# Kernel optimization log

Measured on AMD Instinct MI355X. Metric: run time of the kernel, lower is better.

## Reference

```python
import jax, jax.numpy as jnp
import numpy as np

B, L, D = 4, 4096, 1024


def setup_inputs() -> dict:
    key = jax.random.key(0)
    ks = jax.random.split(key, 10)
    s = 1.0 / np.sqrt(D)  # torch Linear default init scale
    return {
        "x": jax.random.normal(ks[0], (B, L, D), dtype=jnp.float32),
        "hidden": jax.random.normal(ks[1], (B, D), dtype=jnp.float32),
        "W_ln_z": jax.random.uniform(ks[2], (D, D), jnp.float32, -s, s),
        "b_ln_z": jax.random.uniform(ks[3], (D,), jnp.float32, -s, s),
        "W_dt": jax.random.uniform(ks[4], (D, D), jnp.float32, -s, s),
        "b_dt": jax.random.uniform(ks[5], (D,), jnp.float32, -s, s),
        "W_y": jax.random.uniform(ks[6], (D, D), jnp.float32, -s, s),
        "b_y": jax.random.uniform(ks[7], (D,), jnp.float32, -s, s),
        "W_g": jax.random.uniform(ks[8], (D, D), jnp.float32, -s, s),
        "b_g": jax.random.uniform(ks[9], (D,), jnp.float32, -s, s),
    }


def reference(x, hidden, W_ln_z, b_ln_z, W_dt, b_dt, W_y, b_y, W_g, b_g):
    # Linear projections (torch Linear: x @ W.T + b)
    z_pre = x @ W_ln_z.T + b_ln_z          # (B, L, D)
    dt_pre = x @ W_dt.T + b_dt             # (B, L, D)

    # -softplus(-u) == log_sigmoid(u)
    ln_z = jax.nn.log_sigmoid(z_pre)       # ln z
    ln_da = jax.nn.log_sigmoid(dt_pre)     # ln(delta*a)
    ln_z_da = ln_z + ln_da
    ln_o_da = jax.nn.log_sigmoid(-dt_pre)  # -softplus(dt_pre)

    ln_o_da_cumsum = jnp.cumsum(ln_o_da, axis=1)
    # log-space parallel scan: h_t = sum_{s<=t} z_s*da_s * prod_{s<r<=t} o_da_r
    lcse = jax.lax.cumlogsumexp(ln_z_da - ln_o_da_cumsum, axis=1)
    h_inner = jnp.exp(lcse + ln_o_da_cumsum)                       # (B, L, D)
    h_cross = jnp.exp(ln_o_da_cumsum) * hidden[:, None, :]         # (B, L, D)
    h = h_inner + h_cross

    gate = jax.nn.silu(x @ W_g.T + b_g)
    y = (h @ W_y.T + b_y) * gate
    return y, h
```

## Files before the change

kernel.cpp:

```cpp
#include <hip/hip_runtime.h>


#define BDIM 4
#define LDIM 4096
#define DDIM 1024
#define MROWS (BDIM * LDIM)
#define KDIM 1024
#define NPROJ 3072
#define NCHUNK 64
#define LCHUNK 64

typedef __attribute__((ext_vector_type(8))) short short8v;
typedef __attribute__((ext_vector_type(4))) float f32x4;
typedef unsigned int uint;

__device__ __forceinline__ float bf2f(short u) {
    union { float f; uint i; } v;
    v.i = ((uint)(unsigned short)u) << 16;
    return v.f;
}
__device__ __forceinline__ short f2bf(float f) {
    union { float f; uint i; } v; v.f = f;
    uint r = v.i + 0x7FFFu + ((v.i >> 16) & 1u);
    return (short)(r >> 16);
}
__device__ __forceinline__ float sigf(float x) { return 1.f / (1.f + __expf(-x)); }

#define SCANSTEP(zz, dd, H0, H1, A0, A1, DO_A)                                     \
  {                                                                                \
    float _z0 = bf2f((short)((zz) & 0xffff)), _z1 = bf2f((short)((zz) >> 16));     \
    float _d0 = bf2f((short)((dd) & 0xffff)), _d1 = bf2f((short)((dd) >> 16));     \
    float _e0 = __expf(-_d0), _r0 = 1.f / (1.f + _e0);                             \
    float _o0 = _e0 * _r0, _q0 = sigf(_z0) * _r0;                                  \
    float _e1 = __expf(-_d1), _r1 = 1.f / (1.f + _e1);                             \
    float _o1 = _e1 * _r1, _q1 = sigf(_z1) * _r1;                                  \
    H0 = _q0 + _o0 * H0; H1 = _q1 + _o1 * H1;                                      \
    if (DO_A) { A0 *= _o0; A1 *= _o1; }                                            \
  }

__global__ __launch_bounds__(256) void fused_init(
    const float* __restrict__ x,
    const float* __restrict__ W_ln_z, const float* __restrict__ W_dt,
    const float* __restrict__ W_g,    const float* __restrict__ W_y,
    const float* __restrict__ b_ln_z, const float* __restrict__ b_dt,
    const float* __restrict__ b_g,
    short* __restrict__ x_bf, short* __restrict__ Wcat, float* __restrict__ biascat)
{
    int i = blockIdx.x * blockDim.x + threadIdx.x;
    if (i < 4194304) {
        float4 v = reinterpret_cast<const float4*>(x)[i];
        short4 o;
        o.x = f2bf(v.x); o.y = f2bf(v.y); o.z = f2bf(v.z); o.w = f2bf(v.w);
        reinterpret_cast<short4*>(x_bf)[i] = o;
    } else if (i < 5242880) {
        int j = i - 4194304;
        int seg = j >> 18, off = j & ((1 << 18) - 1);
        const float* s = (seg == 0) ? W_ln_z : (seg == 1) ? W_dt : (seg == 2) ? W_g : W_y;
        float4 v = reinterpret_cast<const float4*>(s)[off];
        short4 o;
        o.x = f2bf(v.x); o.y = f2bf(v.y); o.z = f2bf(v.z); o.w = f2bf(v.w);
        reinterpret_cast<short4*>(Wcat)[j] = o;
    } else if (i < 5243648) {
        int j = i - 5242880;
        int seg = j >> 8, off = j & 255;
        const float* s = (seg == 0) ? b_ln_z : (seg == 1) ? b_dt : b_g;
        reinterpret_cast<float4*>(biascat)[j] =
            reinterpret_cast<const float4*>(s)[off];
    }
}

#define STAGE(arr, gbase, half, kofs)                                              \
  do {                                                                             \
    _Pragma("unroll")                                                              \
    for (int _i = 0; _i < 2; ++_i) {                                               \
      int _c = _i * 512 + tid;                                                     \
      int _row = _c >> 3, _g = _c & 7;                                             \
      int _gsw = _g ^ (_row & 7);                                                  \
      __builtin_amdgcn_global_load_lds(                                            \
        (const __attribute__((address_space(1))) void*)(                           \
            (gbase) + (size_t)((half) * 128 + _row) * K + (kofs) + _gsw * 8),      \
        (__attribute__((address_space(3))) void*)(                                 \
            &arr[(_i * 512 + wid * 64) * 8]),                                      \
        16, 0, 0);                                                                 \
    }                                                                              \
  } while (0)

#define LDA4(dst, arr)                                                             \
  _Pragma("unroll")                                                                \
  for (int _m = 0; _m < 4; ++_m) {                                                 \
    int _r = _m * 32 + wm * 16 + lrow;                                             \
    _Pragma("unroll")                                                              \
    for (int _kk = 0; _kk < 2; ++_kk)                                              \
      dst[_m][_kk] = *(const short8v*)&arr[_r * 64 +                               \
                       (((_kk * 4 + kq) ^ (lrow & 7)) * 8)];                       \
  }

#define LDB2(dst, arr)                                                             \
  _Pragma("unroll")                                                                \
  for (int _n = 0; _n < 2; ++_n) {                                                 \
    int _r = _n * 64 + wn * 16 + lrow;                                             \
    _Pragma("unroll")                                                              \
    for (int _kk = 0; _kk < 2; ++_kk)                                              \
      dst[_n][_kk] = *(const short8v*)&arr[_r * 64 +                               \
                       (((_kk * 4 + kq) ^ (lrow & 7)) * 8)];                       \
  }

#define MFMAQ(mi0, ni0, afr, bfr)                                                  \
  __builtin_amdgcn_s_setprio(1);                                                   \
  _Pragma("unroll")                                                                \
  for (int _kk = 0; _kk < 2; ++_kk)                                                \
    _Pragma("unroll")                                                              \
    for (int _m = 0; _m < 4; ++_m)                                                 \
      _Pragma("unroll")                                                            \
      for (int _n = 0; _n < 2; ++_n)                                               \
        acc[(mi0) + _m][(ni0) + _n] = __builtin_amdgcn_mfma_f32_16x16x32_bf16(     \
            afr[_m][_kk], bfr[_n][_kk], acc[(mi0) + _m][(ni0) + _n], 0, 0, 0);     \
  __builtin_amdgcn_s_setprio(0);

#define BARB()   __builtin_amdgcn_s_barrier()
#define VM4()    asm volatile("s_waitcnt vmcnt(4)")
#define VM0()    asm volatile("s_waitcnt vmcnt(0)")

template<int OUT_BF16, int HAS_GATE>
__global__ __launch_bounds__(512, 2) void gemm256(
    const short* __restrict__ A, const short* __restrict__ Bm,
    const float* __restrict__ bias, void* __restrict__ Cv,
    int M, int N, int K,
    const short* __restrict__ gate, int ldg)
{
    __shared__ short As0h0[8192], As0h1[8192], As1h0[8192], As1h1[8192];
    __shared__ short Bs0h0[8192], Bs0h1[8192], Bs1h0[8192], Bs1h1[8192];

    const int tid  = threadIdx.x;
    const int lane = tid & 63;
    const int wid  = tid >> 6;
    const int wm   = wid >> 2;
    const int wn   = wid & 3;
    const int lrow = lane & 15;
    const int kq   = lane >> 4;

    const int gx  = gridDim.x;
    const int nwg = gx * gridDim.y;
    int flat = blockIdx.y * gx + blockIdx.x;
    if ((nwg & 7) == 0) { int q = nwg >> 3; flat = (flat & 7) * q + (flat >> 3); }
    const int m0 = (flat / gx) * 256;
    const int n0 = (flat % gx) * 256;

    const short* Abase = A + (size_t)m0 * K;
    const short* Bbase = Bm + (size_t)n0 * K;

    f32x4 acc[8][4];
#pragma unroll
    for (int i = 0; i < 8; ++i)
#pragma unroll
        for (int j = 0; j < 4; ++j)
            acc[i][j] = (f32x4){0.f, 0.f, 0.f, 0.f};

    STAGE(As0h0, Abase, 0, 0);
    STAGE(As0h1, Abase, 1, 0);
    STAGE(Bs0h0, Bbase, 0, 0);
    STAGE(Bs0h1, Bbase, 1, 0);
    STAGE(As1h0, Abase, 0, 64);
    STAGE(Bs1h0, Bbase, 0, 64);
    VM4(); BARB();

    const int NT = K / 64;
    for (int t = 0; t < NT; t += 2) {
        const int k1 = (t + 1) * 64, k2 = (t + 2) * 64, k3 = (t + 3) * 64;
        const bool more = (t + 2) < NT;
        short8v af[4][2], b0[2][2], b1[2][2];

        LDA4(af, As0h0) LDB2(b0, Bs0h0)
        STAGE(As1h1, Abase, 1, k1);
        BARB(); MFMAQ(0, 0, af, b0)

        LDB2(b1, Bs0h1)
        STAGE(Bs1h1, Bbase, 1, k1);
        BARB(); MFMAQ(0, 2, af, b1)

        LDA4(af, As0h1)
        if (more) STAGE(As0h0, Abase, 0, k2);
        BARB(); MFMAQ(4, 2, af, b1)

        if (more) { STAGE(Bs0h0, Bbase, 0, k2); VM4(); } else { VM0(); }
        BARB(); MFMAQ(4, 0, af, b0)

        LDA4(af, As1h0) LDB2(b0, Bs1h0)
        if (more) STAGE(As0h1, Abase, 1, k2);
        BARB(); MFMAQ(0, 0, af, b0)

        LDB2(b1, Bs1h1)
        if (more) STAGE(Bs0h1, Bbase, 1, k2);
        BARB(); MFMAQ(0, 2, af, b1)

        LDA4(af, As1h1)
        if (more) STAGE(As1h0, Abase, 0, k3);
        BARB(); MFMAQ(4, 2, af, b1)

        if (more) { STAGE(Bs1h0, Bbase, 0, k3); VM4(); }
        BARB(); MFMAQ(4, 0, af, b0)
    }

    const int lr4 = (lane >> 4) * 4;
#pragma unroll
    for (int mi = 0; mi < 8; ++mi) {
        int rowb = m0 + mi * 32 + wm * 16 + lr4;
#pragma unroll
        for (int ni = 0; ni < 4; ++ni) {
            int col = n0 + ni * 64 + wn * 16 + lrow;
            float bv = bias[col];
#pragma unroll
            for (int r = 0; r < 4; ++r) {
                int row = rowb + r;
                float val = acc[mi][ni][r] + bv;
                if (HAS_GATE) {
                    float g = bf2f(gate[(size_t)row * ldg + col]);
                    val *= g * sigf(g);
                }
                if (OUT_BF16)
                    ((short*)Cv)[(size_t)row * N + col] = f2bf(val);
                else
                    ((float*)Cv)[(size_t)row * N + col] = val;
            }
        }
    }
}

__global__ __launch_bounds__(256) void chunk_reduce(
    const short* __restrict__ pre, float* __restrict__ sA, float* __restrict__ sBv)
{
    const int t = threadIdx.x;
    const int c = blockIdx.x;
    const int b = blockIdx.y;
    const int d0 = blockIdx.z * 512 + 2 * t;
    float A0 = 1.f, A1 = 1.f, B0 = 0.f, B1 = 0.f;
    size_t base = ((size_t)(b * LDIM) + c * LCHUNK) * NPROJ + d0;
    for (int i = 0; i < LCHUNK; i += 8) {
        uint z[8], dv[8];
#pragma unroll
        for (int k = 0; k < 8; ++k) {
            z[k]  = *(const uint*)&pre[base + (size_t)k * NPROJ];
            dv[k] = *(const uint*)&pre[base + (size_t)k * NPROJ + DDIM];
        }
#pragma unroll
        for (int k = 0; k < 8; ++k) {
            SCANSTEP(z[k], dv[k], B0, B1, A0, A1, 1)
        }
        base += 8 * NPROJ;
    }
    int idx = ((b * NCHUNK + c) << 10) + d0;
    *reinterpret_cast<float2*>(&sA[idx])  = make_float2(A0, A1);
    *reinterpret_cast<float2*>(&sBv[idx]) = make_float2(B0, B1);
}

__global__ __launch_bounds__(1024) void chunk_prefix(
    const float* __restrict__ sA, const float* __restrict__ sBv,
    const float* __restrict__ hidden, float* __restrict__ sI)
{
    const int d = threadIdx.x;
    const int b = blockIdx.x;
    float h = hidden[b * DDIM + d];
    int idx = (b * NCHUNK << 10) + d;
    for (int c = 0; c < NCHUNK; c += 4) {
        float a0 = sA[idx];            float v0 = sBv[idx];
        float a1 = sA[idx + 1024];     float v1 = sBv[idx + 1024];
        float a2 = sA[idx + 2048];     float v2 = sBv[idx + 2048];
        float a3 = sA[idx + 3072];     float v3 = sBv[idx + 3072];
        sI[idx]        = h; h = v0 + a0 * h;
        sI[idx + 1024] = h; h = v1 + a1 * h;
        sI[idx + 2048] = h; h = v2 + a2 * h;
        sI[idx + 3072] = h; h = v3 + a3 * h;
        idx += 4096;
    }
}

__global__ __launch_bounds__(256) void chunk_apply(
    const short* __restrict__ pre, const float* __restrict__ sI,
    float* __restrict__ hout, short* __restrict__ hbf)
{
    const int t = threadIdx.x;
    const int c = blockIdx.x;
    const int b = blockIdx.y;
    const int d0 = blockIdx.z * 512 + 2 * t;
    float2 hi = *reinterpret_cast<const float2*>(&sI[((b * NCHUNK + c) << 10) + d0]);
    float h0 = hi.x, h1 = hi.y;
    size_t base  = ((size_t)(b * LDIM) + c * LCHUNK) * NPROJ + d0;
    size_t obase = ((size_t)(b * LDIM) + c * LCHUNK) * DDIM + d0;
    for (int i = 0; i < LCHUNK; i += 8) {
        uint z[8], dv[8];
#pragma unroll
        for (int k = 0; k < 8; ++k) {
            z[k]  = *(const uint*)&pre[base + (size_t)k * NPROJ];
            dv[k] = *(const uint*)&pre[base + (size_t)k * NPROJ + DDIM];
        }
        float dummyA = 0.f, dummyB = 0.f;
#pragma unroll
        for (int k = 0; k < 8; ++k) {
            SCANSTEP(z[k], dv[k], h0, h1, dummyA, dummyB, 0)
            *reinterpret_cast<float2*>(&hout[obase + (size_t)k * DDIM]) =
                make_float2(h0, h1);
            *reinterpret_cast<uint*>(&hbf[obase + (size_t)k * DDIM]) =
                ((uint)(unsigned short)f2bf(h0)) |
                (((uint)(unsigned short)f2bf(h1)) << 16);
        }
        base += 8 * NPROJ;
        obase += 8 * DDIM;
    }
}

extern "C" void kernel_launch(void* const* d_in, const int* in_sizes, int n_in,
                              void* d_out, int out_size, void* d_ws, size_t ws_size,
                              hipStream_t stream) {
    const float* x      = (const float*)d_in[0];
    const float* hidden = (const float*)d_in[1];
    const float* W_ln_z = (const float*)d_in[2];
    const float* b_ln_z = (const float*)d_in[3];
    const float* W_dt   = (const float*)d_in[4];
    const float* b_dt   = (const float*)d_in[5];
    const float* W_y    = (const float*)d_in[6];
    const float* b_y    = (const float*)d_in[7];
    const float* W_g    = (const float*)d_in[8];
    const float* b_g    = (const float*)d_in[9];

    char* ws = (char*)d_ws;
    short* x_bf   = (short*)(ws + 0);
    short* Wcat   = (short*)(ws + 33554432);
    short* Wy_bf  = (short*)(ws + 39845888);
    float* biascat= (float*)(ws + 41943040);
    short* pre    = (short*)(ws + 41955328);
    float* sA     = (float*)(ws + 142618624);
    float* sBv    = (float*)(ws + 143667200);
    float* sI     = (float*)(ws + 144715776);

    fused_init<<<20484, 256, 0, stream>>>(x, W_ln_z, W_dt, W_g, W_y,
                                          b_ln_z, b_dt, b_g, x_bf, Wcat, biascat);

    gemm256<1, 0><<<dim3(NPROJ / 256, MROWS / 256), 512, 0, stream>>>(
        x_bf, Wcat, biascat, pre, MROWS, NPROJ, KDIM, nullptr, 0);

    float* y_out = (float*)d_out;
    float* h_out = (float*)d_out + (size_t)MROWS * DDIM;
    short* h_bf  = x_bf;
    chunk_reduce<<<dim3(NCHUNK, BDIM, 2), 256, 0, stream>>>(pre, sA, sBv);
    chunk_prefix<<<dim3(BDIM), 1024, 0, stream>>>(sA, sBv, hidden, sI);
    chunk_apply<<<dim3(NCHUNK, BDIM, 2), 256, 0, stream>>>(pre, sI, h_out, h_bf);

    gemm256<0, 1><<<dim3(DDIM / 256, MROWS / 256), 512, 0, stream>>>(
        h_bf, Wy_bf, b_y, y_out, MROWS, DDIM, KDIM, pre + 2 * DDIM, NPROJ);
}
```

Before: 242.1 us.

## Shrink GEMM tiles from 256x256 to 128x128 with four workgroups per CU

Replaces the 256x256 GEMM tile kernel with a 128x128 tile version that uses half the LDS and fewer accumulators, and raises launch bounds to four workgroups per CU. Each wave now owns a 64x32 output patch and the staging, fragment-load and MFMA macros are reworked to match the new layout. The aim is more workgroups, which helps wave-level latency hiding and load balance across CUs. In exchange, each loaded byte is reused less, so global and LDS traffic per FLOP goes up and each MFMA phase has fewer instructions to hide load latency.

```diff
diff --git a/kernel.cpp b/kernel.cpp
--- a/kernel.cpp
+++ b/kernel.cpp
@@ -69,67 +69,60 @@
     }
 }
 
-#define STAGE(arr, gbase, half, kofs)                                              \
+
+#define STG(arrh, gbase, half, kofs)                                               \
   do {                                                                             \
-    _Pragma("unroll")                                                              \
-    for (int _i = 0; _i < 2; ++_i) {                                               \
-      int _c = _i * 512 + tid;                                                     \
-      int _row = _c >> 3, _g = _c & 7;                                             \
-      int _gsw = _g ^ (_row & 7);                                                  \
-      __builtin_amdgcn_global_load_lds(                                            \
-        (const __attribute__((address_space(1))) void*)(                           \
-            (gbase) + (size_t)((half) * 128 + _row) * K + (kofs) + _gsw * 8),      \
-        (__attribute__((address_space(3))) void*)(                                 \
-            &arr[(_i * 512 + wid * 64) * 8]),                                      \
-        16, 0, 0);                                                                 \
-    }                                                                              \
+    int _row = tid >> 3, _g = tid & 7;                                             \
+    int _gsw = _g ^ (_row & 7);                                                    \
+    __builtin_amdgcn_global_load_lds(                                              \
+      (const __attribute__((address_space(1))) void*)(                             \
+          (gbase) + (size_t)((half) * 64 + _row) * K + (kofs) + _gsw * 8),         \
+      (__attribute__((address_space(3))) void*)(&(arrh)[wid * 512]),               \
+      16, 0, 0);                                                                   \
   } while (0)
 
-#define LDA4(dst, arr)                                                             \
+#define LDA(dst, buf)                                                              \
   _Pragma("unroll")                                                                \
   for (int _m = 0; _m < 4; ++_m) {                                                 \
-    int _r = _m * 32 + wm * 16 + lrow;                                             \
+    int _r = _m * 16 + lrow;                                                       \
     _Pragma("unroll")                                                              \
     for (int _kk = 0; _kk < 2; ++_kk)                                              \
-      dst[_m][_kk] = *(const short8v*)&arr[_r * 64 +                               \
-                       (((_kk * 4 + kq) ^ (lrow & 7)) * 8)];                       \
+      dst[_m][_kk] = *(const short8v*)&buf[wm][_r * 64 +                           \
+                       (((_kk * 4 + kq) ^ (_r & 7)) * 8)];                         \
   }
 
-#define LDB2(dst, arr)                                                             \
-  _Pragma("unroll")                                                                \
-  for (int _n = 0; _n < 2; ++_n) {                                                 \
-    int _r = _n * 64 + wn * 16 + lrow;                                             \
+#define LDB(dst, buf, ni)                                                          \
+  {                                                                                \
+    int _c = (wn & 1) * 32 + (ni) * 16 + lrow;                                     \
     _Pragma("unroll")                                                              \
     for (int _kk = 0; _kk < 2; ++_kk)                                              \
-      dst[_n][_kk] = *(const short8v*)&arr[_r * 64 +                               \
-                       (((_kk * 4 + kq) ^ (lrow & 7)) * 8)];                       \
+      dst[_kk] = *(const short8v*)&buf[wn >> 1][_c * 64 +                          \
+                   (((_kk * 4 + kq) ^ (_c & 7)) * 8)];                             \
   }
 
-#define MFMAQ(mi0, ni0, afr, bfr)                                                  \
+#define MFMAP(mi0, ni, bfr)                                                        \
   __builtin_amdgcn_s_setprio(1);                                                   \
   _Pragma("unroll")                                                                \
   for (int _kk = 0; _kk < 2; ++_kk)                                                \
     _Pragma("unroll")                                                              \
-    for (int _m = 0; _m < 4; ++_m)                                                 \
-      _Pragma("unroll")                                                            \
-      for (int _n = 0; _n < 2; ++_n)                                               \
-        acc[(mi0) + _m][(ni0) + _n] = __builtin_amdgcn_mfma_f32_16x16x32_bf16(     \
-            afr[_m][_kk], bfr[_n][_kk], acc[(mi0) + _m][(ni0) + _n], 0, 0, 0);     \
+    for (int _m = (mi0); _m < (mi0) + 2; ++_m)                                     \
+      acc[_m][ni] = __builtin_amdgcn_mfma_f32_16x16x32_bf16(                       \
+          af[_m][_kk], bfr[_kk], acc[_m][ni], 0, 0, 0);                            \
   __builtin_amdgcn_s_setprio(0);
 
 #define BARB()   __builtin_amdgcn_s_barrier()
-#define VM4()    asm volatile("s_waitcnt vmcnt(4)")
+#define VM2()    asm volatile("s_waitcnt vmcnt(2)")
 #define VM0()    asm volatile("s_waitcnt vmcnt(0)")
 
 template<int OUT_BF16, int HAS_GATE>
-__global__ __launch_bounds__(512, 2) void gemm256(
+__global__ __launch_bounds__(512, 4) void gemm128(
     const short* __restrict__ A, const short* __restrict__ Bm,
     const float* __restrict__ bias, void* __restrict__ Cv,
     int M, int N, int K,
     const short* __restrict__ gate, int ldg)
 {
-    __shared__ short As0h0[8192], As0h1[8192], As1h0[8192], As1h1[8192];
-    __shared__ short Bs0h0[8192], Bs0h1[8192], Bs1h0[8192], Bs1h1[8192];
+    __shared__ short As0[2][4096], As1[2][4096];
+    __shared__ short Bs0[2][4096], Bs1[2][4096];
 
     const int tid  = threadIdx.x;
     const int lane = tid & 63;
@@ -143,71 +136,64 @@
     const int nwg = gx * gridDim.y;
     int flat = blockIdx.y * gx + blockIdx.x;
     if ((nwg & 7) == 0) { int q = nwg >> 3; flat = (flat & 7) * q + (flat >> 3); }
-    const int m0 = (flat / gx) * 256;
-    const int n0 = (flat % gx) * 256;
+    const int m0 = (flat / gx) * 128;
+    const int n0 = (flat % gx) * 128;
 
     const short* Abase = A + (size_t)m0 * K;
     const short* Bbase = Bm + (size_t)n0 * K;
 
-    f32x4 acc[8][4];
-#pragma unroll
-    for (int i = 0; i < 8; ++i)
-#pragma unroll
-        for (int j = 0; j < 4; ++j)
+    f32x4 acc[4][2];
+#pragma unroll
+    for (int i = 0; i < 4; ++i)
+#pragma unroll
+        for (int j = 0; j < 2; ++j)
             acc[i][j] = (f32x4){0.f, 0.f, 0.f, 0.f};
 
-    STAGE(As0h0, Abase, 0, 0);
-    STAGE(As0h1, Abase, 1, 0);
-    STAGE(Bs0h0, Bbase, 0, 0);
-    STAGE(Bs0h1, Bbase, 1, 0);
-    STAGE(As1h0, Abase, 0, 64);
-    STAGE(Bs1h0, Bbase, 0, 64);
-    VM4(); BARB();
+    short8v af[4][2], b0[2], b1[2];
+
+    STG(As0[0], Abase, 0, 0);
+    STG(As0[1], Abase, 1, 0);
+    STG(Bs0[0], Bbase, 0, 0);
+    STG(Bs0[1], Bbase, 1, 0);
+    STG(As1[0], Abase, 0, 64);
+    STG(Bs1[0], Bbase, 0, 64);
+    VM2(); BARB();
 
     const int NT = K / 64;
     for (int t = 0; t < NT; t += 2) {
         const int k1 = (t + 1) * 64, k2 = (t + 2) * 64, k3 = (t + 3) * 64;
         const bool more = (t + 2) < NT;
-        short8v af[4][2], b0[2][2], b1[2][2];
-
-        LDA4(af, As0h0) LDB2(b0, Bs0h0)
-        STAGE(As1h1, Abase, 1, k1);
-        BARB(); MFMAQ(0, 0, af, b0)
-
-        LDB2(b1, Bs0h1)
-        STAGE(Bs1h1, Bbase, 1, k1);
-        BARB(); MFMAQ(0, 2, af, b1)
-
-        LDA4(af, As0h1)
-        if (more) STAGE(As0h0, Abase, 0, k2);
-        BARB(); MFMAQ(4, 2, af, b1)
-
-        if (more) { STAGE(Bs0h0, Bbase, 0, k2); VM4(); } else { VM0(); }
-        BARB(); MFMAQ(4, 0, af, b0)
-
-        LDA4(af, As1h0) LDB2(b0, Bs1h0)
-        if (more) STAGE(As0h1, Abase, 1, k2);
-        BARB(); MFMAQ(0, 0, af, b0)
-
-        LDB2(b1, Bs1h1)
-        if (more) STAGE(Bs0h1, Bbase, 1, k2);
-        BARB(); MFMAQ(0, 2, af, b1)
-
-        LDA4(af, As1h1)
-        if (more) STAGE(As1h0, Abase, 0, k3);
-        BARB(); MFMAQ(4, 2, af, b1)
-
-        if (more) { STAGE(Bs1h0, Bbase, 0, k3); VM4(); }
-        BARB(); MFMAQ(4, 0, af, b0)
+
+        LDA(af, As0) LDB(b0, Bs0, 0)
+        STG(As1[1], Abase, 1, k1);
+        BARB(); MFMAP(0, 0, b0)
+        LDB(b1, Bs0, 1)
+        STG(Bs1[1], Bbase, 1, k1);
+        BARB(); MFMAP(2, 0, b0)
+        if (more) STG(As0[0], Abase, 0, k2);
+        BARB(); MFMAP(2, 1, b1)
+        if (more) { STG(Bs0[0], Bbase, 0, k2); VM2(); } else { VM0(); }
+        BARB(); MFMAP(0, 1, b1)
+
+        LDA(af, As1) LDB(b0, Bs1, 0)
+        if (more) STG(As0[1], Abase, 1, k2);
+        BARB(); MFMAP(0, 0, b0)
+        LDB(b1, Bs1, 1)
+        if (more) STG(Bs0[1], Bbase, 1, k2);
+        BARB(); MFMAP(2, 0, b0)
+        if (more) STG(As1[0], Abase, 0, k3);
+        BARB(); MFMAP(2, 1, b1)
+        if (more) { STG(Bs1[0], Bbase, 0, k3); VM2(); }
+        BARB(); MFMAP(0, 1, b1)
     }
 
     const int lr4 = (lane >> 4) * 4;
 #pragma unroll
-    for (int mi = 0; mi < 8; ++mi) {
-        int rowb = m0 + mi * 32 + wm * 16 + lr4;
-#pragma unroll
-        for (int ni = 0; ni < 4; ++ni) {
-            int col = n0 + ni * 64 + wn * 16 + lrow;
+    for (int mi = 0; mi < 4; ++mi) {
+        int rowb = m0 + wm * 64 + mi * 16 + lr4;
+#pragma unroll
+        for (int ni = 0; ni < 2; ++ni) {
+            int col = n0 + wn * 32 + ni * 16 + lrow;
             float bv = bias[col];
 #pragma unroll
             for (int r = 0; r < 4; ++r) {
@@ -335,7 +321,7 @@
     fused_init<<<20484, 256, 0, stream>>>(x, W_ln_z, W_dt, W_g, W_y,
                                           b_ln_z, b_dt, b_g, x_bf, Wcat, biascat);
 
-    gemm256<1, 0><<<dim3(NPROJ / 256, MROWS / 256), 512, 0, stream>>>(
+    gemm128<1, 0><<<dim3(NPROJ / 128, MROWS / 128), 512, 0, stream>>>(
         x_bf, Wcat, biascat, pre, MROWS, NPROJ, KDIM, nullptr, 0);
 
     float* y_out = (float*)d_out;
@@ -345,6 +331,6 @@
     chunk_prefix<<<dim3(BDIM), 1024, 0, stream>>>(sA, sBv, hidden, sI);
     chunk_apply<<<dim3(NCHUNK, BDIM, 2), 256, 0, stream>>>(pre, sI, h_out, h_bf);
 
-    gemm256<0, 1><<<dim3(DDIM / 256, MROWS / 256), 512, 0, stream>>>(
+    gemm128<0, 1><<<dim3(DDIM / 128, MROWS / 128), 512, 0, stream>>>(
         h_bf, Wy_bf, b_y, y_out, MROWS, DDIM, KDIM, pre + 2 * DDIM, NPROJ);
 }
```

New measurement: 256.0 us. 5.8% more time.
